# Kernel optimization log

Hardware: AMD Instinct MI355X
Metric: run time of the kernel (lower is better)

## Reference

```python
import jax, jax.numpy as jnp
import numpy as np

N = 100_000      # nodes
E = 1_600_000    # edges
D = 128          # hidden_channels
L = 3            # num_layers
G = 5_000        # number of subgraphs (batch ids)
MAXZ = 1_000     # max_z


def setup_inputs() -> dict:
    key = jax.random.key(0)
    ks = jax.random.split(key, 8)
    s = 1.0 / np.sqrt(D)
    return {
        "z": jax.random.randint(ks[0], (N,), 0, MAXZ, dtype=jnp.int32),
        "edge_index": jax.random.randint(ks[1], (2, E), 0, N, dtype=jnp.int32),
        # sorted graph ids, G segments of equal size (each subgraph has >=2 nodes)
        "batch": (jnp.arange(N) * G // N).astype(jnp.int32),
        "z_table": jax.random.normal(ks[2], (MAXZ, D), dtype=jnp.float32) * s,
        "Wl": jax.random.normal(ks[3], (L, D, D), dtype=jnp.float32) * s,
        "bl": jnp.zeros((L, D), jnp.float32),
        "Wr": jax.random.normal(ks[4], (L, D, D), dtype=jnp.float32) * s,
        "W1": jax.random.normal(ks[5], (D, D), dtype=jnp.float32) * s,
        "b1": jnp.zeros((D,), jnp.float32),
        "W2": jax.random.normal(ks[6], (1, D), dtype=jnp.float32) * s,
        "b2": jnp.zeros((1,), jnp.float32),
    }


def reference(z, edge_index, batch, z_table, Wl, bl, Wr, W1, b1, W2, b2):
    src, dst = edge_index[0], edge_index[1]
    x = z_table[z]  # [N, D] z-label embedding (use_feature=False, no node_embedding)

    # in-degree for mean aggregation (shared across layers)
    counts = jax.ops.segment_sum(jnp.ones((E,), x.dtype), dst, num_segments=N)
    inv_deg = 1.0 / jnp.maximum(counts, 1.0)  # [N]

    for l in range(L):
        # SAGEConv: mean-aggregate neighbor features, then lin_l(agg) + lin_r(x)
        agg = jax.ops.segment_sum(x[src], dst, num_segments=N) * inv_deg[:, None]
        x = agg @ Wl[l].T + bl[l] + x @ Wr[l].T
        if l < L - 1:
            x = jax.nn.relu(x)  # dropout is identity in eval mode

    # first node index of each sorted batch segment (np.unique return_index equiv.)
    centers = jnp.searchsorted(batch, jnp.arange(G))  # [G]
    h = x[centers] * x[centers + 1]                   # pairwise center product
    h = jax.nn.relu(h @ W1.T + b1)
    return h @ W2.T + b2  # [G, 1]
```

## Files before the change

kernel.cpp:

```cpp
#include <hip/hip_runtime.h>
#include <hip/hip_bf16.h>
#include <hip/hip_fp16.h>

#define D 128
#define NL 3
#define NODE_SH 8
#define NB_MAX 512
#define BIN_CHUNK 4096

typedef __attribute__((ext_vector_type(8))) short short8;
typedef __attribute__((ext_vector_type(4))) float f32x4;

static inline size_t align256(size_t x){ return (x + 255) & ~(size_t)255; }

static __device__ inline unsigned short f2bf_hi(float f){
    __hip_bfloat16 h = __float2bfloat16(f);
    return *reinterpret_cast<unsigned short*>(&h);
}
static __device__ inline float bf2f(unsigned short u){
    return __uint_as_float(((unsigned)u) << 16);
}

__global__ __launch_bounds__(256) void k_embed(const int* __restrict__ z, const float* __restrict__ zt,
                                               float* __restrict__ x, __half* __restrict__ xh, int N){
    int i = blockIdx.x * blockDim.x + threadIdx.x;
    int n = i >> 5, q = i & 31;
    if (n >= N) return;
    float4 v = *(const float4*)&zt[(size_t)z[n] * D + q * 4];
    *(float4*)&x[(size_t)n * D + q * 4] = v;
    __half2 p0 = __floats2half2_rn(v.x, v.y);
    __half2 p1 = __floats2half2_rn(v.z, v.w);
    uint2 u;
    u.x = *reinterpret_cast<unsigned*>(&p0);
    u.y = *reinterpret_cast<unsigned*>(&p1);
    *(uint2*)&xh[(size_t)n * D + q * 4] = u;
}

__global__ __launch_bounds__(256) void k_deg(const int* __restrict__ dst, int* __restrict__ deg, int E){
    int e = blockIdx.x * blockDim.x + threadIdx.x;
    if (e < E) atomicAdd(&deg[dst[e]], 1);
}

__global__ __launch_bounds__(256) void k_invdeg(const int* __restrict__ deg, float* __restrict__ invdeg, int N){
    int n = blockIdx.x * blockDim.x + threadIdx.x;
    if (n < N) invdeg[n] = 1.0f / (float)max(deg[n], 1);
}

#define SCAN_B 512
__global__ __launch_bounds__(SCAN_B) void k_scan1(const int* __restrict__ deg, int* __restrict__ bsum, int N){
    __shared__ int s[SCAN_B];
    int i = blockIdx.x * SCAN_B + threadIdx.x;
    s[threadIdx.x] = (i < N) ? deg[i] : 0;
    __syncthreads();
    for (int st = SCAN_B / 2; st > 0; st >>= 1){
        if (threadIdx.x < st) s[threadIdx.x] += s[threadIdx.x + st];
        __syncthreads();
    }
    if (threadIdx.x == 0) bsum[blockIdx.x] = s[0];
}

__global__ __launch_bounds__(SCAN_B) void k_scan2(int* __restrict__ bsum, int nb){
    __shared__ int s[SCAN_B];
    int t = threadIdx.x;
    int v = (t < nb) ? bsum[t] : 0;
    s[t] = v; __syncthreads();
    for (int st = 1; st < SCAN_B; st <<= 1){
        int u = (t >= st) ? s[t - st] : 0;
        __syncthreads();
        s[t] += u;
        __syncthreads();
    }
    if (t < nb) bsum[t] = s[t] - v;
}

__global__ __launch_bounds__(SCAN_B) void k_scan3(const int* __restrict__ deg, const int* __restrict__ bsum,
                                                  int* __restrict__ offs, int N, int E){
    __shared__ int s[SCAN_B];
    int i = blockIdx.x * SCAN_B + threadIdx.x;
    int v = (i < N) ? deg[i] : 0;
    s[threadIdx.x] = v; __syncthreads();
    for (int st = 1; st < SCAN_B; st <<= 1){
        int u = (threadIdx.x >= st) ? s[threadIdx.x - st] : 0;
        __syncthreads();
        s[threadIdx.x] += u;
        __syncthreads();
    }
    if (i < N) offs[i] = s[threadIdx.x] - v + bsum[blockIdx.x];
    if (blockIdx.x == 0 && threadIdx.x == 0) offs[N] = E;
}

__global__ __launch_bounds__(256) void k_bcur(const int* __restrict__ offs, int* __restrict__ gcur,
                                              int NB, int N){
    int b = blockIdx.x * blockDim.x + threadIdx.x;
    if (b < NB) gcur[b] = offs[min(b << NODE_SH, N)];
}

__global__ __launch_bounds__(256) void k_binA(const int* __restrict__ src, const int* __restrict__ dst,
                                              int* __restrict__ gcur, int* __restrict__ ebuf2,
                                              int E, int NB){
    __shared__ int s_hist[NB_MAX];
    __shared__ int s_lofs[NB_MAX];
    __shared__ int s_delta[NB_MAX];
    __shared__ int s_pack[BIN_CHUNK];
    __shared__ int s_gdst[BIN_CHUNK];
    __shared__ int s_scan[256];
    const int t = threadIdx.x;
    const int e0 = blockIdx.x * BIN_CHUNK;
    for (int b = t; b < NB_MAX; b += 256) s_hist[b] = 0;
    __syncthreads();
    int my_pack[16], my_b[16], my_rank[16];
    #pragma unroll
    for (int i = 0; i < 16; ++i){
        int e = e0 + i * 256 + t;
        if (e < E){
            int s = src[e], d = dst[e];
            int b = d >> NODE_SH;
            my_pack[i] = s | ((d & 255) << 17);
            my_b[i] = b;
            my_rank[i] = atomicAdd(&s_hist[b], 1);
        } else my_b[i] = -1;
    }
    __syncthreads();
    int h0 = s_hist[2 * t], h1 = s_hist[2 * t + 1];
    int sum2 = h0 + h1;
    s_scan[t] = sum2;
    __syncthreads();
    for (int st = 1; st < 256; st <<= 1){
        int v = (t >= st) ? s_scan[t - st] : 0;
        __syncthreads();
        s_scan[t] += v;
        __syncthreads();
    }
    int excl = s_scan[t] - sum2;
    s_lofs[2 * t] = excl;
    s_lofs[2 * t + 1] = excl + h0;
    __syncthreads();
    for (int b = t; b < NB; b += 256){
        int h = s_hist[b];
        int base = (h > 0) ? atomicAdd(&gcur[b], h) : 0;
        s_delta[b] = base - s_lofs[b];
    }
    __syncthreads();
    #pragma unroll
    for (int i = 0; i < 16; ++i){
        if (my_b[i] >= 0){
            int j = s_lofs[my_b[i]] + my_rank[i];
            s_pack[j] = my_pack[i];
            s_gdst[j] = j + s_delta[my_b[i]];
        }
    }
    __syncthreads();
    const int cnt = min(BIN_CHUNK, E - e0);
    for (int j = t; j < cnt; j += 256)
        ebuf2[s_gdst[j]] = s_pack[j];
}

__global__ __launch_bounds__(256) void k_binB(const int* __restrict__ ebuf2, const int* __restrict__ offs,
                                              int* __restrict__ ebuf, int N){
    __shared__ int lcur[256];
    const int b = blockIdx.x, t = threadIdx.x;
    const int n0 = b << NODE_SH;
    const int n1 = min(n0 + 256, N);
    if (n0 + t < n1) lcur[t] = offs[n0 + t];
    __syncthreads();
    const int rs = offs[n0], re = offs[n1];
    for (int i = rs + t; i < re; i += 256){
        int v = ebuf2[i];
        int p = atomicAdd(&lcur[v >> 17], 1);
        ebuf[p] = v & 0x1FFFF;
    }
}

__global__ __launch_bounds__(256) void k_centers(const int* __restrict__ batch, int* __restrict__ centers, int N){
    int n = blockIdx.x * blockDim.x + threadIdx.x;
    if (n < N && (n == 0 || batch[n] != batch[n - 1])) centers[batch[n]] = n;
}

__global__ __launch_bounds__(256) void k_prepW(const float* __restrict__ Wl, const float* __restrict__ Wr,
                                               const float* __restrict__ W1, float* __restrict__ W1T,
                                               unsigned short* __restrict__ WFh, unsigned short* __restrict__ WFl){
    int i = blockIdx.x * blockDim.x + threadIdx.x;
    if (i < NL * 8 * 8 * 64){
        int lane = i & 63;
        int r = i >> 6;
        int fn = r & 7; r >>= 3;
        int ks = r & 7; r >>= 3;
        int l = r;
        int col = fn * 16 + (lane & 15);
        int k0 = ks * 32 + (lane >> 4) * 8;
        short8 hh, ll;
        #pragma unroll
        for (int j = 0; j < 8; ++j){
            int k = k0 + j;
            float w = (k < D) ? Wl[(size_t)l * D * D + col * D + k]
                              : Wr[(size_t)l * D * D + col * D + (k - D)];
            unsigned short h = f2bf_hi(w);
            hh[j] = (short)h;
            ll[j] = (short)f2bf_hi(w - bf2f(h));
        }
        *(short8*)&WFh[(size_t)i * 8] = hh;
        *(short8*)&WFl[(size_t)i * 8] = ll;
    }
    if (i < D * D){ int k = i / D, d = i % D; W1T[i] = W1[d * D + k]; }
}

static __device__ inline void acc_h4(float4& a, uint2 u){
    __half2 h0 = *reinterpret_cast<__half2*>(&u.x);
    __half2 h1 = *reinterpret_cast<__half2*>(&u.y);
    float2 f0 = __half22float2(h0);
    float2 f1 = __half22float2(h1);
    a.x += f0.x; a.y += f0.y; a.z += f1.x; a.w += f1.y;
}

__global__ __launch_bounds__(256) void k_agg(const __half* __restrict__ xh, const int* __restrict__ ebuf,
                                             const int* __restrict__ offs, const float* __restrict__ invdeg,
                                             float* __restrict__ agg, int N){
    int node = blockIdx.x * 8 + (threadIdx.x >> 5);
    if (node >= N) return;
    int lane = threadIdx.x & 31;
    int s = offs[node], e = offs[node + 1];
    float4 a0 = make_float4(0.f,0.f,0.f,0.f), a1 = a0, a2 = a0, a3 = a0;
    int i = s;
    for (; i + 4 <= e; i += 4){
        int nb0 = ebuf[i], nb1 = ebuf[i+1], nb2 = ebuf[i+2], nb3 = ebuf[i+3];
        uint2 u0 = *(const uint2*)&xh[(size_t)nb0 * D + lane * 4];
        uint2 u1 = *(const uint2*)&xh[(size_t)nb1 * D + lane * 4];
        uint2 u2 = *(const uint2*)&xh[(size_t)nb2 * D + lane * 4];
        uint2 u3 = *(const uint2*)&xh[(size_t)nb3 * D + lane * 4];
        acc_h4(a0, u0); acc_h4(a1, u1); acc_h4(a2, u2); acc_h4(a3, u3);
    }
    for (; i < e; ++i){
        uint2 u = *(const uint2*)&xh[(size_t)ebuf[i] * D + lane * 4];
        acc_h4(a0, u);
    }
    a0.x += a1.x + a2.x + a3.x;
    a0.y += a1.y + a2.y + a3.y;
    a0.z += a1.z + a2.z + a3.z;
    a0.w += a1.w + a2.w + a3.w;
    float sc = invdeg[node];
    a0.x *= sc; a0.y *= sc; a0.z *= sc; a0.w *= sc;
    *(float4*)&agg[(size_t)node * D + lane * 4] = a0;
}

template<bool RELU>
__global__ __launch_bounds__(256) void k_dense_mfma(const float* __restrict__ Ag, const float* __restrict__ X,
                                                    const unsigned short* __restrict__ WFh,
                                                    const unsigned short* __restrict__ WFl,
                                                    const float* __restrict__ bias,
                                                    float* __restrict__ Out, __half* __restrict__ XhOut, int N){
    const int wave = threadIdx.x >> 6;
    const int lane = threadIdx.x & 63;
    const int l15  = lane & 15;
    const int kg   = lane >> 4;
    const int rbase = blockIdx.x * 128 + wave * 32;

    f32x4 acc[2][8];
    #pragma unroll
    for (int t = 0; t < 2; ++t)
        #pragma unroll
        for (int fn = 0; fn < 8; ++fn) acc[t][fn] = (f32x4){0.f, 0.f, 0.f, 0.f};

    #pragma unroll
    for (int ks = 0; ks < 8; ++ks){
        const float* S = (ks < 4) ? Ag : X;
        const int ko = (ks & 3) * 32 + kg * 8;
        short8 ah[2], al[2];
        #pragma unroll
        for (int t = 0; t < 2; ++t){
            int row = rbase + t * 16 + l15;
            row = min(row, N - 1);
            const float* ap = &S[(size_t)row * D + ko];
            float4 x0 = *(const float4*)ap;
            float4 x1 = *(const float4*)(ap + 4);
            float av[8] = {x0.x, x0.y, x0.z, x0.w, x1.x, x1.y, x1.z, x1.w};
            #pragma unroll
            for (int j = 0; j < 8; ++j){
                unsigned short h = f2bf_hi(av[j]);
                ah[t][j] = (short)h;
                al[t][j] = (short)f2bf_hi(av[j] - bf2f(h));
            }
        }
        #pragma unroll
        for (int fn = 0; fn < 8; ++fn){
            const size_t fo = ((size_t)(ks * 8 + fn) * 64 + lane) * 8;
            const short8 bh = *(const short8*)&WFh[fo];
            const short8 bl = *(const short8*)&WFl[fo];
            #pragma unroll
            for (int t = 0; t < 2; ++t){
                acc[t][fn] = __builtin_amdgcn_mfma_f32_16x16x32_bf16(ah[t], bh, acc[t][fn], 0, 0, 0);
                acc[t][fn] = __builtin_amdgcn_mfma_f32_16x16x32_bf16(al[t], bh, acc[t][fn], 0, 0, 0);
                acc[t][fn] = __builtin_amdgcn_mfma_f32_16x16x32_bf16(ah[t], bl, acc[t][fn], 0, 0, 0);
            }
        }
    }
    #pragma unroll
    for (int t = 0; t < 2; ++t){
        const int rb = rbase + t * 16 + (kg << 2);
        #pragma unroll
        for (int fn = 0; fn < 8; ++fn){
            const int col = fn * 16 + l15;
            const float bv = bias[col];
            #pragma unroll
            for (int r = 0; r < 4; ++r){
                const int orow = rb + r;
                if (orow < N){
                    float v = acc[t][fn][r] + bv;
                    if (RELU) v = fmaxf(v, 0.f);
                    Out[(size_t)orow * D + col] = v;
                    XhOut[(size_t)orow * D + col] = __float2half(v);
                }
            }
        }
    }
}

__global__ __launch_bounds__(128) void k_head(const float* __restrict__ x, const int* __restrict__ centers,
                                              const float* __restrict__ W1T, const float* __restrict__ b1,
                                              const float* __restrict__ W2, const float* __restrict__ b2,
                                              float* __restrict__ out){
    __shared__ float hs[D];
    __shared__ float red[D];
    int g = blockIdx.x; int d = threadIdx.x;
    int c = centers[g];
    hs[d] = x[(size_t)c * D + d] * x[(size_t)(c + 1) * D + d];
    __syncthreads();
    float acc = b1[d];
    #pragma unroll 8
    for (int k = 0; k < D; ++k) acc = fmaf(hs[k], W1T[k * D + d], acc);
    acc = fmaxf(acc, 0.f);
    red[d] = acc * W2[d];
    __syncthreads();
    for (int st = 64; st > 0; st >>= 1){
        if (d < st) red[d] += red[d + st];
        __syncthreads();
    }
    if (d == 0) out[g] = red[0] + b2[0];
}

extern "C" void kernel_launch(void* const* d_in, const int* in_sizes, int n_in,
                              void* d_out, int out_size, void* d_ws, size_t ws_size,
                              hipStream_t stream){
    const int*   z     = (const int*)  d_in[0];
    const int*   eidx  = (const int*)  d_in[1];
    const int*   batch = (const int*)  d_in[2];
    const float* zt    = (const float*)d_in[3];
    const float* Wl    = (const float*)d_in[4];
    const float* bl    = (const float*)d_in[5];
    const float* Wr    = (const float*)d_in[6];
    const float* W1    = (const float*)d_in[7];
    const float* b1    = (const float*)d_in[8];
    const float* W2    = (const float*)d_in[9];
    const float* b2    = (const float*)d_in[10];
    float* out = (float*)d_out;

    const int N = in_sizes[0];
    const int E = in_sizes[1] / 2;
    const int G = out_size;
    const int NB = (N + 255) >> NODE_SH;
    const int* src  = eidx;
    const int* dstp = eidx + E;

    char* p = (char*)d_ws;
    auto alloc = [&](size_t bytes){ char* r = p; p += align256(bytes); return r; };
    float* xa      = (float*)alloc((size_t)N * D * 4);
    float* xb      = (float*)alloc((size_t)N * D * 4);
    float* agg     = (float*)alloc((size_t)N * D * 4);
    __half* xha    = (__half*)alloc((size_t)N * D * 2);
    __half* xhb    = (__half*)alloc((size_t)N * D * 2);
    int*   deg     = (int*)  alloc((size_t)N * 4);
    float* invdeg  = (float*)alloc((size_t)N * 4);
    int*   offs    = (int*)  alloc((size_t)(N + 1) * 4);
    int*   ebuf    = (int*)  alloc((size_t)E * 4);
    int*   ebuf2   = (int*)  alloc((size_t)E * 4);
    int*   centers = (int*)  alloc((size_t)G * 4);
    int*   bsum    = (int*)  alloc((size_t)1024 * 4);
    int*   gcur    = (int*)  alloc((size_t)NB_MAX * 4);
    float* W1T     = (float*)alloc((size_t)D * D * 4);
    unsigned short* WFh = (unsigned short*)alloc((size_t)NL * 8 * 8 * 64 * 8 * 2);
    unsigned short* WFl = (unsigned short*)alloc((size_t)NL * 8 * 8 * 64 * 8 * 2);
    (void)ws_size; (void)n_in;

    hipMemsetAsync(deg, 0, (size_t)N * 4, stream);
    k_embed<<<(N * 32 + 255) / 256, 256, 0, stream>>>(z, zt, xa, xha, N);
    k_deg<<<(E + 255) / 256, 256, 0, stream>>>(dstp, deg, E);
    k_invdeg<<<(N + 255) / 256, 256, 0, stream>>>(deg, invdeg, N);
    int nb1 = (N + SCAN_B - 1) / SCAN_B;
    k_scan1<<<nb1, SCAN_B, 0, stream>>>(deg, bsum, N);
    k_scan2<<<1, SCAN_B, 0, stream>>>(bsum, nb1);
    k_scan3<<<nb1, SCAN_B, 0, stream>>>(deg, bsum, offs, N, E);
    k_bcur<<<(NB + 255) / 256, 256, 0, stream>>>(offs, gcur, NB, N);
    k_binA<<<(E + BIN_CHUNK - 1) / BIN_CHUNK, 256, 0, stream>>>(src, dstp, gcur, ebuf2, E, NB);
    k_binB<<<NB, 256, 0, stream>>>(ebuf2, offs, ebuf, N);
    k_centers<<<(N + 255) / 256, 256, 0, stream>>>(batch, centers, N);
    k_prepW<<<64, 256, 0, stream>>>(Wl, Wr, W1, W1T, WFh, WFl);

    float* xc = xa; float* xn = xb;
    __half* xhc = xha; __half* xhn = xhb;
    for (int l = 0; l < NL; ++l){
        k_agg<<<(N + 7) / 8, 256, 0, stream>>>(xhc, ebuf, offs, invdeg, agg, N);
        const unsigned short* wh = WFh + (size_t)l * 8 * 8 * 64 * 8;
        const unsigned short* wl = WFl + (size_t)l * 8 * 8 * 64 * 8;
        if (l < NL - 1)
            k_dense_mfma<true ><<<(N + 127) / 128, 256, 0, stream>>>(agg, xc, wh, wl, bl + l * D, xn, xhn, N);
        else
            k_dense_mfma<false><<<(N + 127) / 128, 256, 0, stream>>>(agg, xc, wh, wl, bl + l * D, xn, xhn, N);
        float* t = xc; xc = xn; xn = t;
        __half* th = xhc; xhc = xhn; xhn = th;
    }
    k_head<<<G, 128, 0, stream>>>(xc, centers, W1T, b1, W2, b2, out);
}
```

Before: 551.2 us.

## Replace per-node degree atomics and scans with coarse bucket counting in CSR build

Replaces the global per-node degree atomics, the three-pass scan and the bucket-cursor kernel with a shared-memory histogram over 256-node buckets and a single-block scan. Per-node degrees, CSR offsets and inverse degrees are then computed inside the second binning pass from local shared-memory counts. This cuts several kernel launches and removes 1.6M global atomics, at the cost of an extra read of the binned edge buffer and an in-block scan in k_binB.

Result: faster. 492.8 us (-10.6%).

```diff
diff --git a/kernel.cpp b/kernel.cpp
--- a/kernel.cpp
+++ b/kernel.cpp
@@ -36,63 +36,41 @@
     *(uint2*)&xh[(size_t)n * D + q * 4] = u;
 }
 
-__global__ __launch_bounds__(256) void k_deg(const int* __restrict__ dst, int* __restrict__ deg, int E){
-    int e = blockIdx.x * blockDim.x + threadIdx.x;
-    if (e < E) atomicAdd(&deg[dst[e]], 1);
-}
-
-__global__ __launch_bounds__(256) void k_invdeg(const int* __restrict__ deg, float* __restrict__ invdeg, int N){
-    int n = blockIdx.x * blockDim.x + threadIdx.x;
-    if (n < N) invdeg[n] = 1.0f / (float)max(deg[n], 1);
-}
-
-#define SCAN_B 512
-__global__ __launch_bounds__(SCAN_B) void k_scan1(const int* __restrict__ deg, int* __restrict__ bsum, int N){
-    __shared__ int s[SCAN_B];
-    int i = blockIdx.x * SCAN_B + threadIdx.x;
-    s[threadIdx.x] = (i < N) ? deg[i] : 0;
-    __syncthreads();
-    for (int st = SCAN_B / 2; st > 0; st >>= 1){
-        if (threadIdx.x < st) s[threadIdx.x] += s[threadIdx.x + st];
-        __syncthreads();
-    }
-    if (threadIdx.x == 0) bsum[blockIdx.x] = s[0];
-}
-
-__global__ __launch_bounds__(SCAN_B) void k_scan2(int* __restrict__ bsum, int nb){
-    __shared__ int s[SCAN_B];
+__global__ __launch_bounds__(256) void k_bcount(const int* __restrict__ dst, int* __restrict__ bcnt,
+                                                int E, int NB){
+    __shared__ int h[NB_MAX];
+    const int t = threadIdx.x;
+    for (int b = t; b < NB_MAX; b += 256) h[b] = 0;
+    __syncthreads();
+    const int stride = gridDim.x * 256;
+    for (int e = blockIdx.x * 256 + t; e < E; e += stride)
+        atomicAdd(&h[dst[e] >> NODE_SH], 1);
+    __syncthreads();
+    for (int b = t; b < NB; b += 256){
+        int v = h[b];
+        if (v) atomicAdd(&bcnt[b], v);
+    }
+}
+
+__global__ __launch_bounds__(512) void k_bscan(const int* __restrict__ bcnt, int* __restrict__ gbase,
+                                               int* __restrict__ gcur, int* __restrict__ offs,
+                                               int NB, int N, int E){
+    __shared__ int s[512];
     int t = threadIdx.x;
-    int v = (t < nb) ? bsum[t] : 0;
+    int v = (t < NB) ? bcnt[t] : 0;
     s[t] = v; __syncthreads();
-    for (int st = 1; st < SCAN_B; st <<= 1){
+    for (int st = 1; st < 512; st <<= 1){
         int u = (t >= st) ? s[t - st] : 0;
         __syncthreads();
         s[t] += u;
         __syncthreads();
     }
-    if (t < nb) bsum[t] = s[t] - v;
-}
-
-__global__ __launch_bounds__(SCAN_B) void k_scan3(const int* __restrict__ deg, const int* __restrict__ bsum,
-                                                  int* __restrict__ offs, int N, int E){
-    __shared__ int s[SCAN_B];
-    int i = blockIdx.x * SCAN_B + threadIdx.x;
-    int v = (i < N) ? deg[i] : 0;
-    s[threadIdx.x] = v; __syncthreads();
-    for (int st = 1; st < SCAN_B; st <<= 1){
-        int u = (threadIdx.x >= st) ? s[threadIdx.x - st] : 0;
-        __syncthreads();
-        s[threadIdx.x] += u;
-        __syncthreads();
-    }
-    if (i < N) offs[i] = s[threadIdx.x] - v + bsum[blockIdx.x];
-    if (blockIdx.x == 0 && threadIdx.x == 0) offs[N] = E;
-}
-
-__global__ __launch_bounds__(256) void k_bcur(const int* __restrict__ offs, int* __restrict__ gcur,
-                                              int NB, int N){
-    int b = blockIdx.x * blockDim.x + threadIdx.x;
-    if (b < NB) gcur[b] = offs[min(b << NODE_SH, N)];
+    if (t < NB){
+        int base = s[t] - v;
+        gbase[t] = base;
+        gcur[t] = base;
+    }
+    if (t == 0){ gbase[NB] = E; offs[N] = E; }
 }
 
 __global__ __launch_bounds__(256) void k_binA(const int* __restrict__ src, const int* __restrict__ dst,
@@ -155,15 +133,36 @@
         ebuf2[s_gdst[j]] = s_pack[j];
 }
 
-__global__ __launch_bounds__(256) void k_binB(const int* __restrict__ ebuf2, const int* __restrict__ offs,
-                                              int* __restrict__ ebuf, int N){
+__global__ __launch_bounds__(256) void k_binB(const int* __restrict__ ebuf2, const int* __restrict__ gbase,
+                                              int* __restrict__ ebuf, int* __restrict__ offs,
+                                              float* __restrict__ invdeg, int N){
+    __shared__ int cnt[256];
     __shared__ int lcur[256];
+    __shared__ int s_scan[256];
     const int b = blockIdx.x, t = threadIdx.x;
     const int n0 = b << NODE_SH;
-    const int n1 = min(n0 + 256, N);
-    if (n0 + t < n1) lcur[t] = offs[n0 + t];
-    __syncthreads();
-    const int rs = offs[n0], re = offs[n1];
+    const int rs = gbase[b], re = gbase[b + 1];
+    cnt[t] = 0;
+    __syncthreads();
+    for (int i = rs + t; i < re; i += 256)
+        atomicAdd(&cnt[ebuf2[i] >> 17], 1);
+    __syncthreads();
+    const int c = cnt[t];
+    s_scan[t] = c;
+    __syncthreads();
+    for (int st = 1; st < 256; st <<= 1){
+        int u = (t >= st) ? s_scan[t - st] : 0;
+        __syncthreads();
+        s_scan[t] += u;
+        __syncthreads();
+    }
+    const int excl = s_scan[t] - c;
+    lcur[t] = rs + excl;
+    if (n0 + t < N){
+        offs[n0 + t]   = rs + excl;
+        invdeg[n0 + t] = 1.0f / (float)max(c, 1);
+    }
+    __syncthreads();
     for (int i = rs + t; i < re; i += 256){
         int v = ebuf2[i];
         int p = atomicAdd(&lcur[v >> 17], 1);
@@ -367,30 +366,25 @@
     float* agg     = (float*)alloc((size_t)N * D * 4);
     __half* xha    = (__half*)alloc((size_t)N * D * 2);
     __half* xhb    = (__half*)alloc((size_t)N * D * 2);
-    int*   deg     = (int*)  alloc((size_t)N * 4);
     float* invdeg  = (float*)alloc((size_t)N * 4);
     int*   offs    = (int*)  alloc((size_t)(N + 1) * 4);
     int*   ebuf    = (int*)  alloc((size_t)E * 4);
     int*   ebuf2   = (int*)  alloc((size_t)E * 4);
     int*   centers = (int*)  alloc((size_t)G * 4);
-    int*   bsum    = (int*)  alloc((size_t)1024 * 4);
+    int*   bcnt    = (int*)  alloc((size_t)NB_MAX * 4);
+    int*   gbase   = (int*)  alloc((size_t)(NB_MAX + 1) * 4);
     int*   gcur    = (int*)  alloc((size_t)NB_MAX * 4);
     float* W1T     = (float*)alloc((size_t)D * D * 4);
     unsigned short* WFh = (unsigned short*)alloc((size_t)NL * 8 * 8 * 64 * 8 * 2);
     unsigned short* WFl = (unsigned short*)alloc((size_t)NL * 8 * 8 * 64 * 8 * 2);
     (void)ws_size; (void)n_in;
 
-    hipMemsetAsync(deg, 0, (size_t)N * 4, stream);
+    hipMemsetAsync(bcnt, 0, (size_t)NB_MAX * 4, stream);
     k_embed<<<(N * 32 + 255) / 256, 256, 0, stream>>>(z, zt, xa, xha, N);
-    k_deg<<<(E + 255) / 256, 256, 0, stream>>>(dstp, deg, E);
-    k_invdeg<<<(N + 255) / 256, 256, 0, stream>>>(deg, invdeg, N);
-    int nb1 = (N + SCAN_B - 1) / SCAN_B;
-    k_scan1<<<nb1, SCAN_B, 0, stream>>>(deg, bsum, N);
-    k_scan2<<<1, SCAN_B, 0, stream>>>(bsum, nb1);
-    k_scan3<<<nb1, SCAN_B, 0, stream>>>(deg, bsum, offs, N, E);
-    k_bcur<<<(NB + 255) / 256, 256, 0, stream>>>(offs, gcur, NB, N);
+    k_bcount<<<512, 256, 0, stream>>>(dstp, bcnt, E, NB);
+    k_bscan<<<1, 512, 0, stream>>>(bcnt, gbase, gcur, offs, NB, N, E);
     k_binA<<<(E + BIN_CHUNK - 1) / BIN_CHUNK, 256, 0, stream>>>(src, dstp, gcur, ebuf2, E, NB);
-    k_binB<<<NB, 256, 0, stream>>>(ebuf2, offs, ebuf, N);
+    k_binB<<<NB, 256, 0, stream>>>(ebuf2, gbase, ebuf, offs, invdeg, N);
     k_centers<<<(N + 255) / 256, 256, 0, stream>>>(batch, centers, N);
     k_prepW<<<64, 256, 0, stream>>>(Wl, Wr, W1, W1T, WFh, WFl);
 
```
